# Performance work log

Measured on AMD Instinct MI355X. Metric: run time of the kernel, lower is better.

## Reference

```python
import jax, jax.numpy as jnp
import numpy as np

B, QL, VL, HID, NH, CH = 16, 512, 512, 1024, 4, 10
DIM = HID // NH  # 256


def setup_inputs() -> dict:
    key = jax.random.key(0)
    ks = jax.random.split(key, 16)
    n = lambda k, s, sc=0.02: jax.random.normal(k, s, jnp.float32) * sc
    return {
        "query": jax.random.normal(ks[0], (B, QL, HID), jnp.float32),
        "value": jax.random.normal(ks[1], (B, VL, HID), jnp.float32),
        "prev_attn": jax.nn.softmax(jax.random.normal(ks[2], (B * NH, VL), jnp.float32), axis=-1),
        "conv_w": n(ks[3], (CH, 1, 3)),          # conv1d weight (out, in, k)
        "conv_b": jnp.zeros((CH,), jnp.float32),
        "Wq": n(ks[4], (HID, HID)), "bq": jnp.zeros((HID,), jnp.float32),  # query_projection
        "Wv": n(ks[5], (HID, HID)),               # value_projection (no bias)
        "Wloc": n(ks[6], (CH, DIM)),              # loc_projection (no bias)
        "bias": jax.random.uniform(ks[7], (HID,), jnp.float32, -0.1, 0.1),
        "Wout": n(ks[8], (2 * HID, HID)), "bout": jnp.zeros((HID,), jnp.float32),
        "swq": n(ks[9], (DIM, DIM)), "sbq": jnp.zeros((DIM,), jnp.float32),
        "swk": n(ks[10], (DIM, DIM)), "sbk": jnp.zeros((DIM,), jnp.float32),
        "swv": n(ks[11], (DIM, DIM)), "sbv": jnp.zeros((DIM,), jnp.float32),
    }


def _forward(query, value, prev_attn, conv_w, conv_b, Wq, bq, Wv, Wloc, bias,
             Wout, bout, swq, sbq, swk, sbk, swv, sbv):
    # location energy: conv1d over prev alignment, then per-head linear
    conv = jax.lax.conv_general_dilated(
        prev_attn[:, None, :], conv_w, window_strides=(1,), padding=((1, 1),),
        dimension_numbers=("NCH", "OIH", "NCH")) + conv_b[None, :, None]  # (B*NH, CH, VL)
    conv = conv.reshape(B, NH, CH, VL).transpose(0, 1, 3, 2)              # (B, NH, VL, CH)
    loc = jnp.einsum("bhvc,cd->bhvd", conv, Wloc)                         # (B, NH, VL, DIM)
    loc = loc.transpose(0, 2, 1, 3).reshape(B, VL, HID)                   # (B, VL, HID)

    q = query @ Wq + bq                                                   # (B, QL, HID)
    v = value @ Wv + loc + bias                                           # (B, VL, HID)

    # split heads: (B, L, NH, DIM) -> (NH*B, L, DIM)
    qh = q.reshape(B, QL, NH, DIM).transpose(2, 0, 1, 3).reshape(NH * B, QL, DIM)
    vh = v.reshape(B, VL, NH, DIM).transpose(2, 0, 1, 3).reshape(NH * B, VL, DIM)

    # scaled dot-product attention with key = value = vh (intended call)
    qq = qh @ swq + sbq
    kk = vh @ swk + sbk
    vv = vh @ swv + sbv
    scores = jnp.einsum("nqd,nkd->nqk", qq, kk) / np.float32(np.sqrt(DIM))
    attn = jax.nn.softmax(scores, axis=-1)                                # (NH*B, QL, VL)
    ctx = jnp.einsum("nqk,nkd->nqd", attn, vv)

    # merge heads: (NH, B, QL, DIM) -> (B, QL, HID)
    ctx = ctx.reshape(NH, B, QL, DIM).transpose(1, 2, 0, 3).reshape(B, QL, HID)

    combined = jnp.concatenate([ctx, query], axis=2)                      # (B, QL, 2*HID)
    out = jnp.tanh(combined @ Wout + bout)                                # (B, QL, HID)
    return out, attn


def reference(query, value, prev_attn, conv_w, conv_b, Wq, bq, Wv, Wloc, bias,
              Wout, bout, swq, sbq, swk, sbk, swv, sbv):
    return _forward(query, value, prev_attn, conv_w, conv_b, Wq, bq, Wv, Wloc,
                    bias, Wout, bout, swq, sbq, swk, sbk, swv, sbv)
```

## Files before the change

### kernel.cpp

```cpp
#include <hip/hip_runtime.h>
#include <math.h>

#define B_   16
#define QL_  512
#define VL_  512
#define HID_ 1024
#define NH_  4
#define CH_  10
#define DIM_ 256

typedef __attribute__((ext_vector_type(4))) float f32x4;
typedef __attribute__((ext_vector_type(8))) short bf16x8;
typedef long long ll;

__device__ __forceinline__ ushort f2bf(float f) {
    union { float f; uint32_t u; } c; c.f = f;
    uint32_t u = c.u;
    u += 0x7fffu + ((u >> 16) & 1u);
    return (ushort)(u >> 16);
}

__device__ __forceinline__ void gload16(const void* g, void* l) {
    __builtin_amdgcn_global_load_lds((const __attribute__((address_space(1))) void*)g,
                                     (__attribute__((address_space(3))) void*)l,
                                     16, 0, 0);
}

__global__ __launch_bounds__(512)
void gemm8p(const ushort* __restrict__ A, const ushort* __restrict__ Bt,
            void* __restrict__ Cv, void* __restrict__ Cv2,
            const float* __restrict__ bias,
            int K, int lda, int ldb, int ldc,
            float post_scale, int flags)
{
    __shared__ ushort As[2][256 * 32];
    __shared__ ushort Bs[2][128 * 32];

    int gx = gridDim.x, nwg = gx * gridDim.y;
    int flat = blockIdx.y * gx + blockIdx.x;
    int q = nwg >> 3, r = nwg & 7;
    int xcd = flat & 7, idx = flat >> 3;
    int logical = (xcd < r ? xcd * (q + 1) : r * (q + 1) + (xcd - r) * q) + idx;
    int brow = (logical / gx) * 256;
    int bcol = (logical % gx) * 128;

    int t = threadIdx.x;
    int lane = t & 63, w = t >> 6;
    int wm = w >> 1, wn = w & 1;
    int wr = wm * 64, wc = wn * 64;

    int srow = t >> 2, slot = t & 3;
    int sk = ((slot ^ ((srow >> 1) & 3)) << 3);
    const ushort* gA0 = A  + (ll)(brow + srow) * lda + sk;
    const ushort* gA1 = A  + (ll)(brow + 128 + srow) * lda + sk;
    const ushort* gB  = Bt + (ll)(bcol + srow) * ldb + sk;

    f32x4 acc[4][4] = {};

    auto stage = [&](int buf, int k0) {
        gload16(gA0 + k0, &As[buf][t * 8]);
        gload16(gA1 + k0, &As[buf][4096 + t * 8]);
        gload16(gB  + k0, &Bs[buf][t * 8]);
    };

    int NT = K >> 5;
    stage(0, 0);
    __syncthreads();
    int cur = 0;
    int slotR = (lane >> 4) ^ ((lane >> 1) & 3);
    for (int tI = 0; tI < NT; ++tI) {
        const ushort* ab = &As[cur][(wr + (lane & 15)) * 32 + slotR * 8];
        const ushort* bb = &Bs[cur][(wc + (lane & 15)) * 32 + slotR * 8];

        bf16x8 af[4], b0, b1;
        #pragma unroll
        for (int m = 0; m < 4; ++m) af[m] = *(const bf16x8*)(ab + m * 512);
        b0 = *(const bf16x8*)(bb);
        b1 = *(const bf16x8*)(bb + 512);
        if (tI + 1 < NT) stage(cur ^ 1, (tI + 1) << 5);
        __builtin_amdgcn_s_barrier();
        __builtin_amdgcn_sched_barrier(0);
        __builtin_amdgcn_s_setprio(1);
        #pragma unroll
        for (int m = 0; m < 4; ++m) {
            acc[m][0] = __builtin_amdgcn_mfma_f32_16x16x32_bf16(af[m], b0, acc[m][0], 0, 0, 0);
            acc[m][1] = __builtin_amdgcn_mfma_f32_16x16x32_bf16(af[m], b1, acc[m][1], 0, 0, 0);
        }
        __builtin_amdgcn_s_setprio(0);
        __builtin_amdgcn_s_barrier();
        __builtin_amdgcn_sched_barrier(0);

        bf16x8 b2 = *(const bf16x8*)(bb + 1024);
        bf16x8 b3 = *(const bf16x8*)(bb + 1536);
        __builtin_amdgcn_s_setprio(1);
        #pragma unroll
        for (int m = 0; m < 4; ++m) {
            acc[m][2] = __builtin_amdgcn_mfma_f32_16x16x32_bf16(af[m], b2, acc[m][2], 0, 0, 0);
            acc[m][3] = __builtin_amdgcn_mfma_f32_16x16x32_bf16(af[m], b3, acc[m][3], 0, 0, 0);
        }
        __builtin_amdgcn_s_setprio(0);
        if (tI + 1 < NT)
            asm volatile("s_waitcnt vmcnt(0)" ::: "memory");
        __builtin_amdgcn_s_barrier();
        __builtin_amdgcn_sched_barrier(0);
        cur ^= 1;
    }

    float*  Cf = (float*)Cv;
    ushort* Cb = (ushort*)Cv;
    ushort* C2 = (ushort*)Cv2;
    #pragma unroll
    for (int m = 0; m < 4; ++m) {
        int r0 = brow + wr + m * 16 + (lane >> 4) * 4;
        #pragma unroll
        for (int n = 0; n < 4; ++n) {
            int c = bcol + wc + n * 16 + (lane & 15);
            float bv = bias ? bias[c] : 0.0f;
            float v0 = (acc[m][n][0] + bv) * post_scale;
            float v1 = (acc[m][n][1] + bv) * post_scale;
            float v2 = (acc[m][n][2] + bv) * post_scale;
            float v3 = (acc[m][n][3] + bv) * post_scale;
            if (flags & 2) { v0 = tanhf(v0); v1 = tanhf(v1); v2 = tanhf(v2); v3 = tanhf(v3); }
            if ((flags & 8) && c >= 1024) {
                ushort4 o;
                o.x = f2bf(v0); o.y = f2bf(v1); o.z = f2bf(v2); o.w = f2bf(v3);
                *(ushort4*)&C2[(ll)(c - 1024) * 8192 + r0] = o;
            } else if (flags & 1) {
                Cb[(ll)(r0 + 0) * ldc + c] = f2bf(v0);
                Cb[(ll)(r0 + 1) * ldc + c] = f2bf(v1);
                Cb[(ll)(r0 + 2) * ldc + c] = f2bf(v2);
                Cb[(ll)(r0 + 3) * ldc + c] = f2bf(v3);
            } else {
                Cf[(ll)(r0 + 0) * ldc + c] = v0;
                Cf[(ll)(r0 + 1) * ldc + c] = v1;
                Cf[(ll)(r0 + 2) * ldc + c] = v2;
                Cf[(ll)(r0 + 3) * ldc + c] = v3;
            }
        }
    }
}

__global__ __launch_bounds__(256)
void gemm_bf16(const ushort* __restrict__ A, const ushort* __restrict__ Bt,
               void* __restrict__ Cv, void* __restrict__ Cv2,
               const float* __restrict__ bias,
               int K, int lda, int ldb, int ldc,
               long long a1, long long a2, long long b1, long long b2,
               long long c1, long long c2, int WB,
               float post_scale, int flags)
{
    __shared__ ushort As[2][128 * 64];
    __shared__ ushort Bs[2][128 * 64];

    int z = blockIdx.z;
    int zm = z % WB, zd = z / WB;
    A  += a1 * zm + a2 * zd;
    Bt += b1 * zm + b2 * zd;
    long long coff = c1 * (long long)zm + c2 * (long long)zd;

    int gx = gridDim.x;
    int nwg = gx * gridDim.y;
    int flat = blockIdx.y * gx + blockIdx.x;
    int q = nwg >> 3, r = nwg & 7;
    int xcd = flat & 7, idx = flat >> 3;
    int logical = (xcd < r ? xcd * (q + 1) : r * (q + 1) + (xcd - r) * q) + idx;
    int brow = (logical / gx) * 128;
    int bcol = (logical % gx) * 128;

    int t = threadIdx.x;
    int lane = t & 63, w = t >> 6;
    int wr = (w >> 1) * 64, wc = (w & 1) * 64;

    int srow  = t >> 3;
    int sslot = t & 7;
    int sk = ((sslot ^ (srow & 7)) << 3);
    const ushort* gaBase = A  + (long long)(brow + srow) * lda + sk;
    const ushort* gbBase = Bt + (long long)(bcol + srow) * ldb + sk;

    f32x4 acc[4][4] = {};

    auto stage = [&](int buf, int k0) {
        ushort* la = &As[buf][t * 8];
        ushort* lb = &Bs[buf][t * 8];
        #pragma unroll
        for (int i = 0; i < 4; ++i) {
            gload16(gaBase + (long long)(i * 32) * lda + k0, la + i * 2048);
            gload16(gbBase + (long long)(i * 32) * ldb + k0, lb + i * 2048);
        }
    };

    int NT = K >> 6;
    stage(0, 0);
    int cur = 0;
    for (int tI = 0; tI < NT; ++tI) {
        if (tI + 1 < NT) {
            stage(cur ^ 1, (tI + 1) << 6);
            asm volatile("s_waitcnt vmcnt(8)" ::: "memory");
        } else {
            asm volatile("s_waitcnt vmcnt(0)" ::: "memory");
        }
        __builtin_amdgcn_s_barrier();
        __builtin_amdgcn_sched_barrier(0);

        #pragma unroll
        for (int kk = 0; kk < 2; ++kk) {
            int slot = ((kk << 2) + (lane >> 4)) ^ (lane & 7);
            const ushort* ab = &As[cur][(wr + (lane & 15)) * 64 + slot * 8];
            const ushort* bb = &Bs[cur][(wc + (lane & 15)) * 64 + slot * 8];
            bf16x8 af[4], bfr[4];
            #pragma unroll
            for (int m = 0; m < 4; ++m) af[m]  = *(const bf16x8*)(ab + m * 1024);
            #pragma unroll
            for (int n = 0; n < 4; ++n) bfr[n] = *(const bf16x8*)(bb + n * 1024);
            #pragma unroll
            for (int m = 0; m < 4; ++m)
                #pragma unroll
                for (int n = 0; n < 4; ++n)
                    acc[m][n] = __builtin_amdgcn_mfma_f32_16x16x32_bf16(af[m], bfr[n], acc[m][n], 0, 0, 0);
        }

        __builtin_amdgcn_s_barrier();
        __builtin_amdgcn_sched_barrier(0);
        cur ^= 1;
    }

    float*  Cf = (float*)Cv + coff;
    ushort* Cb = (ushort*)Cv + coff;
    ushort* C2 = (ushort*)Cv2;
    #pragma unroll
    for (int m = 0; m < 4; ++m) {
        int r0 = brow + wr + m * 16 + (lane >> 4) * 4;
        #pragma unroll
        for (int n = 0; n < 4; ++n) {
            int c = bcol + wc + n * 16 + (lane & 15);
            float bv = bias ? bias[c] : 0.0f;
            float v0 = (acc[m][n][0] + bv) * post_scale;
            float v1 = (acc[m][n][1] + bv) * post_scale;
            float v2 = (acc[m][n][2] + bv) * post_scale;
            float v3 = (acc[m][n][3] + bv) * post_scale;
            if (flags & 2) { v0 = tanhf(v0); v1 = tanhf(v1); v2 = tanhf(v2); v3 = tanhf(v3); }
            if ((flags & 8) && c >= 1024) {
                ushort4 o;
                o.x = f2bf(v0); o.y = f2bf(v1); o.z = f2bf(v2); o.w = f2bf(v3);
                *(ushort4*)&C2[(long long)(c - 1024) * 8192 + r0] = o;
            } else if (flags & 1) {
                Cb[(long long)(r0 + 0) * ldc + c] = f2bf(v0);
                Cb[(long long)(r0 + 1) * ldc + c] = f2bf(v1);
                Cb[(long long)(r0 + 2) * ldc + c] = f2bf(v2);
                Cb[(long long)(r0 + 3) * ldc + c] = f2bf(v3);
            } else {
                Cf[(long long)(r0 + 0) * ldc + c] = v0;
                Cf[(long long)(r0 + 1) * ldc + c] = v1;
                Cf[(long long)(r0 + 2) * ldc + c] = v2;
                Cf[(long long)(r0 + 3) * ldc + c] = v3;
            }
        }
    }
}

__global__ __launch_bounds__(512, 1)
void scores_softmax(const ushort* __restrict__ qq, const ushort* __restrict__ kk,
                    float* __restrict__ attn, ushort* __restrict__ attnb)
{
    __shared__ ushort As[128 * 32];
    __shared__ ushort Bs[512 * 32];
    __shared__ float redm[4][128];
    __shared__ float reds[4][128];

    int z = blockIdx.z;
    int b = z & 15, h = z >> 4;
    const ushort* Abase = qq + (ll)b * 524288 + h * 256;
    const ushort* Bbase = kk + (ll)b * 524288 + h * 256;
    float*  aout = attn  + (ll)z * 262144;
    ushort* bout = attnb + (ll)z * 262144;

    int brow = blockIdx.y * 128;

    int t = threadIdx.x;
    int lane = t & 63, w = t >> 6;
    int wr = (w >> 2) * 64;
    int wc = (w & 3) * 128;

    int srow = t >> 2, sslot = t & 3;
    int sk = ((sslot ^ ((srow >> 1) & 3)) << 3);
    const ushort* ga = Abase + (ll)(brow + srow) * 1024 + sk;
    const ushort* gb = Bbase + (ll)srow * 1024 + sk;

    f32x4 acc[4][8] = {};

    for (int k0 = 0; k0 < 256; k0 += 32) {
        gload16(ga + k0, &As[t * 8]);
        #pragma unroll
        for (int i = 0; i < 4; ++i)
            gload16(gb + (ll)(i * 128) * 1024 + k0, &Bs[t * 8 + i * 4096]);
        __syncthreads();

        int slot = (lane >> 4) ^ ((lane >> 1) & 3);
        const ushort* ab = &As[(wr + (lane & 15)) * 32 + slot * 8];
        const ushort* bb = &Bs[(wc + (lane & 15)) * 32 + slot * 8];
        bf16x8 af[4], bfr[8];
        #pragma unroll
        for (int m = 0; m < 4; ++m) af[m]  = *(const bf16x8*)(ab + m * 512);
        #pragma unroll
        for (int n = 0; n < 8; ++n) bfr[n] = *(const bf16x8*)(bb + n * 512);
        #pragma unroll
        for (int m = 0; m < 4; ++m)
            #pragma unroll
            for (int n = 0; n < 8; ++n)
                acc[m][n] = __builtin_amdgcn_mfma_f32_16x16x32_bf16(af[m], bfr[n], acc[m][n], 0, 0, 0);
        __syncthreads();
    }

    float rmax[4][4], rinv[4][4];
    #pragma unroll
    for (int m = 0; m < 4; ++m)
        #pragma unroll
        for (int j = 0; j < 4; ++j) {
            float pm = acc[m][0][j];
            #pragma unroll
            for (int n = 1; n < 8; ++n) pm = fmaxf(pm, acc[m][n][j]);
            pm = fmaxf(pm, __shfl_xor(pm, 1));
            pm = fmaxf(pm, __shfl_xor(pm, 2));
            pm = fmaxf(pm, __shfl_xor(pm, 4));
            pm = fmaxf(pm, __shfl_xor(pm, 8));
            if ((lane & 15) == 0)
                redm[w & 3][wr + m * 16 + (lane >> 4) * 4 + j] = pm;
        }
    __syncthreads();
    #pragma unroll
    for (int m = 0; m < 4; ++m)
        #pragma unroll
        for (int j = 0; j < 4; ++j) {
            int row = wr + m * 16 + (lane >> 4) * 4 + j;
            rmax[m][j] = fmaxf(fmaxf(redm[0][row], redm[1][row]),
                               fmaxf(redm[2][row], redm[3][row]));
        }
    #pragma unroll
    for (int m = 0; m < 4; ++m)
        #pragma unroll
        for (int j = 0; j < 4; ++j) {
            float ps = 0.f;
            #pragma unroll
            for (int n = 0; n < 8; ++n) {
                float e = __expf(acc[m][n][j] - rmax[m][j]);
                acc[m][n][j] = e;
                ps += e;
            }
            ps += __shfl_xor(ps, 1);
            ps += __shfl_xor(ps, 2);
            ps += __shfl_xor(ps, 4);
            ps += __shfl_xor(ps, 8);
            if ((lane & 15) == 0)
                reds[w & 3][wr + m * 16 + (lane >> 4) * 4 + j] = ps;
        }
    __syncthreads();
    #pragma unroll
    for (int m = 0; m < 4; ++m)
        #pragma unroll
        for (int j = 0; j < 4; ++j) {
            int row = wr + m * 16 + (lane >> 4) * 4 + j;
            rinv[m][j] = 1.0f / (reds[0][row] + reds[1][row] + reds[2][row] + reds[3][row]);
        }
    #pragma unroll
    for (int m = 0; m < 4; ++m) {
        int r0 = brow + wr + m * 16 + (lane >> 4) * 4;
        #pragma unroll
        for (int n = 0; n < 8; ++n) {
            int c = wc + n * 16 + (lane & 15);
            #pragma unroll
            for (int j = 0; j < 4; ++j) {
                float v = acc[m][n][j] * rinv[m][j];
                aout[(ll)(r0 + j) * 512 + c] = v;
                bout[(ll)(r0 + j) * 512 + c] = f2bf(v);
            }
        }
    }
}

__global__ __launch_bounds__(256)
void prep_acts(const float* __restrict__ query, const float* __restrict__ value,
               const float* __restrict__ prev, const float* __restrict__ cw,
               const float* __restrict__ cb,
               ushort* __restrict__ Acat, ushort* __restrict__ vext)
{
    int bI = blockIdx.x;
    if (bI < 16384) {
        const float* in = (bI < 8192) ? query : value;
        ushort* out = (bI < 8192) ? Acat : vext;
        int ld_out = (bI < 8192) ? 2048 : 1088;
        ll idx = (ll)(bI & 8191) * 256 + threadIdx.x;
        ll row = idx >> 8;
        int c4 = (int)(idx & 255) * 4;
        float4 v = *(const float4*)&in[row * 1024 + c4];
        ushort4 o;
        o.x = f2bf(v.x); o.y = f2bf(v.y); o.z = f2bf(v.z); o.w = f2bf(v.w);
        *(ushort4*)&out[row * ld_out + c4] = o;
    } else {
        int idx = (bI - 16384) * 256 + threadIdx.x;
        int row = idx >> 6, j = idx & 63;
        int b = row >> 9, l = row & 511;
        ushort v = 0;
        if (j < 40) {
            int h = j / 10, c = j - h * 10;
            const float* p = prev + (ll)(b * 4 + h) * VL_;
            float xm = (l > 0)       ? p[l - 1] : 0.f;
            float x0 = p[l];
            float xp = (l < VL_ - 1) ? p[l + 1] : 0.f;
            v = f2bf(xm * cw[c * 3 + 0] + x0 * cw[c * 3 + 1] + xp * cw[c * 3 + 2] + cb[c]);
        }
        vext[(ll)row * 1088 + 1024 + j] = v;
    }
}

__global__ __launch_bounds__(256)
void prep_w(const float* __restrict__ Wq, const float* __restrict__ Wv,
            ushort* __restrict__ Wqb, ushort* __restrict__ Wvb,
            const float* __restrict__ bq, const float* __restrict__ sbq, const float* __restrict__ swq,
            const float* __restrict__ bias, const float* __restrict__ sbk, const float* __restrict__ swk,
            const float* __restrict__ sbv, const float* __restrict__ swv,
            const float* __restrict__ Wloc,
            float* __restrict__ bqq, float* __restrict__ bkv,
            float* __restrict__ wlK, float* __restrict__ wlV)
{
    int bI = blockIdx.x;
    if (bI < 2048) {
        const float* in = (bI < 1024) ? Wq : Wv;
        ushort* out = (bI < 1024) ? Wqb : Wvb;
        ll idx = (ll)(bI & 1023) * 256 + threadIdx.x;
        ll row = idx >> 8;
        int c4 = (int)(idx & 255) * 4;
        float4 v = *(const float4*)&in[row * 1024 + c4];
        ushort4 o;
        o.x = f2bf(v.x); o.y = f2bf(v.y); o.z = f2bf(v.z); o.w = f2bf(v.w);
        *(ushort4*)&out[row * 1024 + c4] = o;
        return;
    }
    int idx = (bI - 2048) * 256 + threadIdx.x;
    if (idx < 1024) {
        int h = idx >> 8, d = idx & 255;
        float s = 0.f;
        for (int j = 0; j < 256; ++j) s += bq[h * 256 + j] * swq[j * 256 + d];
        bqq[idx] = s + sbq[d];
    } else if (idx < 3072) {
        int i = idx - 1024;
        int kv = i >> 10, ii = i & 1023;
        int h = ii >> 8, d = ii & 255;
        const float* sw = kv ? swv : swk;
        const float* sb = kv ? sbv : sbk;
        float s = 0.f;
        for (int j = 0; j < 256; ++j) s += bias[h * 256 + j] * sw[j * 256 + d];
        bkv[i] = s + sb[d];
    } else if (idx < 5632) {
        int i = idx - 3072; int c = i >> 8, d = i & 255;
        float s = 0.f;
        for (int j = 0; j < 256; ++j) s += Wloc[c * 256 + j] * swk[j * 256 + d];
        wlK[i] = s;
    } else if (idx < 8192) {
        int i = idx - 5632; int c = i >> 8, d = i & 255;
        float s = 0.f;
        for (int j = 0; j < 256; ++j) s += Wloc[c * 256 + j] * swv[j * 256 + d];
        wlV[i] = s;
    }
}

__global__ __launch_bounds__(256)
void transpose_cast(const float* __restrict__ in, ushort* __restrict__ out, int R, int C, int ld_out)
{
    __shared__ float tile[64][65];
    int r0 = blockIdx.y * 64, c0 = blockIdx.x * 64;
    int t = threadIdx.x;
    int tr = t >> 2, tc = (t & 3) * 16;
    const float* ip = in + (ll)(r0 + tr) * C + c0 + tc;
    #pragma unroll
    for (int i = 0; i < 4; ++i) {
        float4 v = *(const float4*)(ip + i * 4);
        tile[tr][tc + i * 4 + 0] = v.x;
        tile[tr][tc + i * 4 + 1] = v.y;
        tile[tr][tc + i * 4 + 2] = v.z;
        tile[tr][tc + i * 4 + 3] = v.w;
    }
    __syncthreads();
    int cl = t >> 2, rl = (t & 3) * 16;
    ushort* op = out + (ll)(c0 + cl) * ld_out + r0 + rl;
    #pragma unroll
    for (int i = 0; i < 16; ++i) op[i] = f2bf(tile[rl + i][cl]);
}

__global__ __launch_bounds__(256)
void sw3_transpose(const float* __restrict__ swq, const float* __restrict__ swk,
                   const float* __restrict__ swv, ushort* __restrict__ oq,
                   ushort* __restrict__ ok, ushort* __restrict__ ov)
{
    __shared__ float tile[64][65];
    const float* in = (blockIdx.z == 0) ? swq : (blockIdx.z == 1) ? swk : swv;
    ushort* out     = (blockIdx.z == 0) ? oq  : (blockIdx.z == 1) ? ok  : ov;
    int r0 = blockIdx.y * 64, c0 = blockIdx.x * 64;
    int t = threadIdx.x;
    int tr = t >> 2, tc = (t & 3) * 16;
    const float* ip = in + (ll)(r0 + tr) * 256 + c0 + tc;
    #pragma unroll
    for (int i = 0; i < 4; ++i) {
        float4 v = *(const float4*)(ip + i * 4);
        tile[tr][tc + i * 4 + 0] = v.x;
        tile[tr][tc + i * 4 + 1] = v.y;
        tile[tr][tc + i * 4 + 2] = v.z;
        tile[tr][tc + i * 4 + 3] = v.w;
    }
    __syncthreads();
    int cl = t >> 2, rl = (t & 3) * 16;
    ushort* op = out + (ll)(c0 + cl) * 256 + r0 + rl;
    #pragma unroll
    for (int i = 0; i < 16; ++i) op[i] = f2bf(tile[rl + i][cl]);
}

__global__ __launch_bounds__(256)
void btext_fill(const float* __restrict__ wlK, const float* __restrict__ wlV,
                ushort* __restrict__ btExt)
{
    int idx = blockIdx.x * 256 + threadIdx.x;
    int n = idx >> 6, j = idx & 63;
    ushort v = 0;
    if (j < 40) {
        int hp = j / 10, c = j - hp * 10;
        int nn = n & 1023;
        int h = nn >> 8, d = nn & 255;
        if (hp == h) {
            const float* wl = (n >= 1024) ? wlV : wlK;
            v = f2bf(wl[c * 256 + d]);
        }
    }
    btExt[(ll)n * 1088 + 1024 + j] = v;
}

extern "C" void kernel_launch(void* const* d_in, const int* in_sizes, int n_in,
                              void* d_out, int out_size, void* d_ws, size_t ws_size,
                              hipStream_t stream)
{
    (void)in_sizes; (void)n_in; (void)out_size; (void)ws_size;

    const float* query = (const float*)d_in[0];
    const float* value = (const float*)d_in[1];
    const float* prev  = (const float*)d_in[2];
    const float* convw = (const float*)d_in[3];
    const float* convb = (const float*)d_in[4];
    const float* Wq    = (const float*)d_in[5];
    const float* bq    = (const float*)d_in[6];
    const float* Wv    = (const float*)d_in[7];
    const float* Wloc  = (const float*)d_in[8];
    const float* bias  = (const float*)d_in[9];
    const float* Wout  = (const float*)d_in[10];
    const float* bout  = (const float*)d_in[11];
    const float* swq   = (const float*)d_in[12];
    const float* sbq   = (const float*)d_in[13];
    const float* swk   = (const float*)d_in[14];
    const float* sbk   = (const float*)d_in[15];
    const float* swv   = (const float*)d_in[16];
    const float* sbv   = (const float*)d_in[17];

    float* out_buf  = (float*)d_out;
    float* attn_buf = out_buf + (ll)B_ * QL_ * HID_;

    char* wsb = (char*)d_ws;
    ushort* vext   = (ushort*)(wsb + 0);
    ushort* WoutTb = (ushort*)(wsb + 0);
    ushort* kkb    = (ushort*)(wsb + 17825792);
    ushort* attnb  = (ushort*)(wsb + 34603008);
    ushort* Acat   = (ushort*)(wsb + 68157440);
    ushort* qqb    = (ushort*)(wsb + 101711872);
    ushort* vvT_b  = (ushort*)(wsb + 118489088);
    float*  bqq    = (float*)(wsb + 135266304);
    float*  bkv    = (float*)(wsb + 135270400);
    float*  wlK    = (float*)(wsb + 135278592);
    float*  wlV    = (float*)(wsb + 135288832);
    ushort* swqTb  = (ushort*)(wsb + 135299072);
    ushort* swkTb  = (ushort*)(wsb + 135430144);
    ushort* swvTb  = (ushort*)(wsb + 135561216);
    ushort* Wqb    = (ushort*)(wsb + 135692288);
    ushort* Wvb    = (ushort*)(wsb + 137789440);
    ushort* wqqTb  = (ushort*)(wsb + 139886592);
    ushort* btExt  = (ushort*)(wsb + 141983744);

    prep_acts<<<18432, 256, 0, stream>>>(query, value, prev, convw, convb, Acat + 1024, vext);
    prep_w<<<2080, 256, 0, stream>>>(Wq, Wv, Wqb, Wvb, bq, sbq, swq, bias, sbk, swk,
                                     sbv, swv, Wloc, bqq, bkv, wlK, wlV);
    sw3_transpose<<<dim3(4, 4, 3), 256, 0, stream>>>(swq, swk, swv, swqTb, swkTb, swvTb);

    gemm_bf16<<<dim3(8, 2, 4), 256, 0, stream>>>(swqTb, Wqb, wqqTb, nullptr, nullptr,
        256, 256, 1024, 1024, 0, 0, 0, 256, 0, 262144, 1, 1.0f, 1);
    gemm_bf16<<<dim3(8, 2, 8), 256, 0, stream>>>(swkTb, Wvb, btExt, nullptr, nullptr,
        256, 256, 1024, 1088, 0, 65536, 256, 0, 278528, 1114112, 4, 1.0f, 1);
    btext_fill<<<512, 256, 0, stream>>>(wlK, wlV, btExt);

    gemm8p<<<dim3(8, 32), 512, 0, stream>>>(Acat + 1024, wqqTb, qqb, nullptr, bqq,
        1024, 2048, 1024, 1024, 0.0625f, 1);

    gemm8p<<<dim3(16, 32), 512, 0, stream>>>(vext, btExt, kkb, vvT_b, bkv,
        1088, 1088, 1088, 1024, 1.0f, 1 | 8);

    transpose_cast<<<dim3(16, 32), 256, 0, stream>>>(Wout, WoutTb, 2048, 1024, 2048);

    scores_softmax<<<dim3(1, 4, 64), 512, 0, stream>>>(qqb, kkb, attn_buf, attnb);

    gemm_bf16<<<dim3(2, 4, 64), 256, 0, stream>>>(attnb, vvT_b, Acat, nullptr, nullptr,
        512, 512, 8192, 2048,
        262144, 4194304, 512, 2097152, 1048576, 256, 16, 1.0f, 1);

    gemm8p<<<dim3(8, 32), 512, 0, stream>>>(Acat, WoutTb, out_buf, nullptr, bout,
        2048, 2048, 2048, 1024, 1.0f, 2);
}
```

Before: 273.4 us.

## Enlarge GEMM tiles to 256x256 with K=64 stages and deeper prefetch

Replaces the 256x128, K=32 tile GEMM with a 256x256 tile using K=64 per stage, an 8-slot XOR swizzle, and four sub-phases per K step. The next stage's loads are issued before compute, with a partial vmcnt wait so two stages stay in flight. The goal is more operand reuse per LDS load and fewer barriers per FLOP. In exchange it uses 128KB of LDS and twice the accumulator registers, which lowers occupancy and halves the workgroup count (128 for the 1024-wide GEMMs), risking underfilled CUs.

```diff
diff --git a/kernel.cpp b/kernel.cpp
--- a/kernel.cpp
+++ b/kernel.cpp
@@ -27,14 +27,14 @@
 }
 
 __global__ __launch_bounds__(512)
-void gemm8p(const ushort* __restrict__ A, const ushort* __restrict__ Bt,
-            void* __restrict__ Cv, void* __restrict__ Cv2,
-            const float* __restrict__ bias,
-            int K, int lda, int ldb, int ldc,
-            float post_scale, int flags)
-{
-    __shared__ ushort As[2][256 * 32];
-    __shared__ ushort Bs[2][128 * 32];
+void gemm256p(const ushort* __restrict__ A, const ushort* __restrict__ Bt,
+              void* __restrict__ Cv, void* __restrict__ Cv2,
+              const float* __restrict__ bias,
+              int K, int lda, int ldb, int ldc,
+              float post_scale, int flags)
+{
+    __shared__ ushort As[2][256 * 64];
+    __shared__ ushort Bs[2][256 * 64];
 
     int gx = gridDim.x, nwg = gx * gridDim.y;
     int flat = blockIdx.y * gx + blockIdx.x;
@@ -42,67 +42,76 @@
     int xcd = flat & 7, idx = flat >> 3;
     int logical = (xcd < r ? xcd * (q + 1) : r * (q + 1) + (xcd - r) * q) + idx;
     int brow = (logical / gx) * 256;
-    int bcol = (logical % gx) * 128;
+    int bcol = (logical % gx) * 256;
 
     int t = threadIdx.x;
     int lane = t & 63, w = t >> 6;
-    int wm = w >> 1, wn = w & 1;
-    int wr = wm * 64, wc = wn * 64;
-
-    int srow = t >> 2, slot = t & 3;
-    int sk = ((slot ^ ((srow >> 1) & 3)) << 3);
-    const ushort* gA0 = A  + (ll)(brow + srow) * lda + sk;
-    const ushort* gA1 = A  + (ll)(brow + 128 + srow) * lda + sk;
-    const ushort* gB  = Bt + (ll)(bcol + srow) * ldb + sk;
-
-    f32x4 acc[4][4] = {};
+    int wm = w >> 2;
+    int wn = w & 3;
+
+    int srow = t >> 3, sslot = t & 7;
+    int sk = ((sslot ^ (srow & 7)) << 3);
+    const ushort* gaBase = A  + (ll)(brow + srow) * lda + sk;
+    const ushort* gbBase = Bt + (ll)(bcol + srow) * ldb + sk;
+
+    f32x4 acc[8][4] = {};
 
     auto stage = [&](int buf, int k0) {
-        gload16(gA0 + k0, &As[buf][t * 8]);
-        gload16(gA1 + k0, &As[buf][4096 + t * 8]);
-        gload16(gB  + k0, &Bs[buf][t * 8]);
+        #pragma unroll
+        for (int j = 0; j < 4; ++j) {
+            gload16(gaBase + (ll)(j * 64) * lda + k0, &As[buf][j * 4096 + t * 8]);
+            gload16(gbBase + (ll)(j * 64) * ldb + k0, &Bs[buf][j * 4096 + t * 8]);
+        }
     };
 
-    int NT = K >> 5;
+    int NT = K >> 6;
     stage(0, 0);
-    __syncthreads();
     int cur = 0;
-    int slotR = (lane >> 4) ^ ((lane >> 1) & 3);
     for (int tI = 0; tI < NT; ++tI) {
-        const ushort* ab = &As[cur][(wr + (lane & 15)) * 32 + slotR * 8];
-        const ushort* bb = &Bs[cur][(wc + (lane & 15)) * 32 + slotR * 8];
-
-        bf16x8 af[4], b0, b1;
-        #pragma unroll
-        for (int m = 0; m < 4; ++m) af[m] = *(const bf16x8*)(ab + m * 512);
-        b0 = *(const bf16x8*)(bb);
-        b1 = *(const bf16x8*)(bb + 512);
-        if (tI + 1 < NT) stage(cur ^ 1, (tI + 1) << 5);
+        if (tI + 1 < NT) {
+            stage(cur ^ 1, (tI + 1) << 6);
+            asm volatile("s_waitcnt vmcnt(8)" ::: "memory");
+        } else {
+            asm volatile("s_waitcnt vmcnt(0)" ::: "memory");
+        }
         __builtin_amdgcn_s_barrier();
         __builtin_amdgcn_sched_barrier(0);
-        __builtin_amdgcn_s_setprio(1);
-        #pragma unroll
-        for (int m = 0; m < 4; ++m) {
-            acc[m][0] = __builtin_amdgcn_mfma_f32_16x16x32_bf16(af[m], b0, acc[m][0], 0, 0, 0);
-            acc[m][1] = __builtin_amdgcn_mfma_f32_16x16x32_bf16(af[m], b1, acc[m][1], 0, 0, 0);
-        }
-        __builtin_amdgcn_s_setprio(0);
-        __builtin_amdgcn_s_barrier();
-        __builtin_amdgcn_sched_barrier(0);
-
-        bf16x8 b2 = *(const bf16x8*)(bb + 1024);
-        bf16x8 b3 = *(const bf16x8*)(bb + 1536);
-        __builtin_amdgcn_s_setprio(1);
-        #pragma unroll
-        for (int m = 0; m < 4; ++m) {
-            acc[m][2] = __builtin_amdgcn_mfma_f32_16x16x32_bf16(af[m], b2, acc[m][2], 0, 0, 0);
-            acc[m][3] = __builtin_amdgcn_mfma_f32_16x16x32_bf16(af[m], b3, acc[m][3], 0, 0, 0);
-        }
-        __builtin_amdgcn_s_setprio(0);
-        if (tI + 1 < NT)
-            asm volatile("s_waitcnt vmcnt(0)" ::: "memory");
-        __builtin_amdgcn_s_barrier();
-        __builtin_amdgcn_sched_barrier(0);
+
+        #pragma unroll
+        for (int p = 0; p < 4; ++p) {
+            int mq = p >> 1, nq = p & 1;
+            bf16x8 af[4][2], bfr[2][2];
+            #pragma unroll
+            for (int m = 0; m < 4; ++m) {
+                int R = wm * 128 + (mq * 4 + m) * 16 + (lane & 15);
+                #pragma unroll
+                for (int kf = 0; kf < 2; ++kf) {
+                    int g = kf * 4 + (lane >> 4);
+                    af[m][kf] = *(const bf16x8*)&As[cur][R * 64 + ((g ^ (lane & 7)) << 3)];
+                }
+            }
+            #pragma unroll
+            for (int n = 0; n < 2; ++n) {
+                int C = wn * 64 + (nq * 2 + n) * 16 + (lane & 15);
+                #pragma unroll
+                for (int kf = 0; kf < 2; ++kf) {
+                    int g = kf * 4 + (lane >> 4);
+                    bfr[n][kf] = *(const bf16x8*)&Bs[cur][C * 64 + ((g ^ (lane & 7)) << 3)];
+                }
+            }
+            __builtin_amdgcn_s_setprio(1);
+            #pragma unroll
+            for (int m = 0; m < 4; ++m)
+                #pragma unroll
+                for (int n = 0; n < 2; ++n)
+                    #pragma unroll
+                    for (int kf = 0; kf < 2; ++kf)
+                        acc[mq * 4 + m][nq * 2 + n] = __builtin_amdgcn_mfma_f32_16x16x32_bf16(
+                            af[m][kf], bfr[n][kf], acc[mq * 4 + m][nq * 2 + n], 0, 0, 0);
+            __builtin_amdgcn_s_setprio(0);
+            __builtin_amdgcn_s_barrier();
+            __builtin_amdgcn_sched_barrier(0);
+        }
         cur ^= 1;
     }
 
@@ -110,16 +119,16 @@
     ushort* Cb = (ushort*)Cv;
     ushort* C2 = (ushort*)Cv2;
     #pragma unroll
-    for (int m = 0; m < 4; ++m) {
-        int r0 = brow + wr + m * 16 + (lane >> 4) * 4;
-        #pragma unroll
-        for (int n = 0; n < 4; ++n) {
-            int c = bcol + wc + n * 16 + (lane & 15);
+    for (int mi = 0; mi < 8; ++mi) {
+        int r0 = brow + wm * 128 + mi * 16 + (lane >> 4) * 4;
+        #pragma unroll
+        for (int ni = 0; ni < 4; ++ni) {
+            int c = bcol + wn * 64 + ni * 16 + (lane & 15);
             float bv = bias ? bias[c] : 0.0f;
-            float v0 = (acc[m][n][0] + bv) * post_scale;
-            float v1 = (acc[m][n][1] + bv) * post_scale;
-            float v2 = (acc[m][n][2] + bv) * post_scale;
-            float v3 = (acc[m][n][3] + bv) * post_scale;
+            float v0 = (acc[mi][ni][0] + bv) * post_scale;
+            float v1 = (acc[mi][ni][1] + bv) * post_scale;
+            float v2 = (acc[mi][ni][2] + bv) * post_scale;
+            float v3 = (acc[mi][ni][3] + bv) * post_scale;
             if (flags & 2) { v0 = tanhf(v0); v1 = tanhf(v1); v2 = tanhf(v2); v3 = tanhf(v3); }
             if ((flags & 8) && c >= 1024) {
                 ushort4 o;
@@ -591,10 +600,10 @@
         256, 256, 1024, 1088, 0, 65536, 256, 0, 278528, 1114112, 4, 1.0f, 1);
     btext_fill<<<512, 256, 0, stream>>>(wlK, wlV, btExt);
 
-    gemm8p<<<dim3(8, 32), 512, 0, stream>>>(Acat + 1024, wqqTb, qqb, nullptr, bqq,
+    gemm256p<<<dim3(4, 32), 512, 0, stream>>>(Acat + 1024, wqqTb, qqb, nullptr, bqq,
         1024, 2048, 1024, 1024, 0.0625f, 1);
 
-    gemm8p<<<dim3(16, 32), 512, 0, stream>>>(vext, btExt, kkb, vvT_b, bkv,
+    gemm256p<<<dim3(8, 32), 512, 0, stream>>>(vext, btExt, kkb, vvT_b, bkv,
         1088, 1088, 1088, 1024, 1.0f, 1 | 8);
 
     transpose_cast<<<dim3(16, 32), 256, 0, stream>>>(Wout, WoutTb, 2048, 1024, 2048);
@@ -605,6 +614,6 @@
         512, 512, 8192, 2048,
         262144, 4194304, 512, 2097152, 1048576, 256, 16, 1.0f, 1);
 
-    gemm8p<<<dim3(8, 32), 512, 0, stream>>>(Acat, WoutTb, out_buf, nullptr, bout,
+    gemm256p<<<dim3(4, 32), 512, 0, stream>>>(Acat, WoutTb, out_buf, nullptr, bout,
         2048, 2048, 2048, 1024, 1.0f, 2);
 }
```

New measurement: 343.3 us. +25.5%, slower.

## Shrink GEMM tiles to 128x128 and double-buffer scores kernel with prefetch

Applied to the files above, without the earlier changes.

Replaces the 256x128, 8-wave gemm8p kernel with a 128x128, 4-wave gemm32 variant. The new kernel issues the next K-tile's global-to-LDS loads before computing the current one, waiting with a partial vmcnt, and drops the split-phase MFMA scheduling and setprio hints. The scores_softmax kernel gains double-buffered LDS so the next tile's loads overlap the current MFMAs. This trades larger-tile data reuse for twice as many workgroups and more overlap, and it doubles LDS use in scores_softmax.

```diff
diff --git a/kernel.cpp b/kernel.cpp
--- a/kernel.cpp
+++ b/kernel.cpp
@@ -26,14 +26,14 @@
                                      16, 0, 0);
 }
 
-__global__ __launch_bounds__(512)
-void gemm8p(const ushort* __restrict__ A, const ushort* __restrict__ Bt,
+__global__ __launch_bounds__(256)
+void gemm32(const ushort* __restrict__ A, const ushort* __restrict__ Bt,
             void* __restrict__ Cv, void* __restrict__ Cv2,
             const float* __restrict__ bias,
             int K, int lda, int ldb, int ldc,
             float post_scale, int flags)
 {
-    __shared__ ushort As[2][256 * 32];
+    __shared__ ushort As[2][128 * 32];
     __shared__ ushort Bs[2][128 * 32];
 
     int gx = gridDim.x, nwg = gx * gridDim.y;
@@ -41,66 +41,56 @@
     int q = nwg >> 3, r = nwg & 7;
     int xcd = flat & 7, idx = flat >> 3;
     int logical = (xcd < r ? xcd * (q + 1) : r * (q + 1) + (xcd - r) * q) + idx;
-    int brow = (logical / gx) * 256;
+    int brow = (logical / gx) * 128;
     int bcol = (logical % gx) * 128;
 
     int t = threadIdx.x;
     int lane = t & 63, w = t >> 6;
-    int wm = w >> 1, wn = w & 1;
-    int wr = wm * 64, wc = wn * 64;
-
-    int srow = t >> 2, slot = t & 3;
-    int sk = ((slot ^ ((srow >> 1) & 3)) << 3);
-    const ushort* gA0 = A  + (ll)(brow + srow) * lda + sk;
-    const ushort* gA1 = A  + (ll)(brow + 128 + srow) * lda + sk;
-    const ushort* gB  = Bt + (ll)(bcol + srow) * ldb + sk;
+    int wr = (w >> 1) * 64, wc = (w & 1) * 64;
+
+    int srow = t >> 2, sslot = t & 3;
+    int sk = ((sslot ^ ((srow >> 1) & 3)) << 3);
+    const ushort* gaBase = A  + (ll)(brow + srow) * lda + sk;
+    const ushort* gbBase = Bt + (ll)(bcol + srow) * ldb + sk;
 
     f32x4 acc[4][4] = {};
 
     auto stage = [&](int buf, int k0) {
-        gload16(gA0 + k0, &As[buf][t * 8]);
-        gload16(gA1 + k0, &As[buf][4096 + t * 8]);
-        gload16(gB  + k0, &Bs[buf][t * 8]);
+        ushort* la = &As[buf][t * 8];
+        ushort* lb = &Bs[buf][t * 8];
+        gload16(gaBase + k0, la);
+        gload16(gaBase + (ll)64 * lda + k0, la + 2048);
+        gload16(gbBase + k0, lb);
+        gload16(gbBase + (ll)64 * ldb + k0, lb + 2048);
     };
 
     int NT = K >> 5;
     stage(0, 0);
-    __syncthreads();
     int cur = 0;
     int slotR = (lane >> 4) ^ ((lane >> 1) & 3);
     for (int tI = 0; tI < NT; ++tI) {
+        if (tI + 1 < NT) {
+            stage(cur ^ 1, (tI + 1) << 5);
+            asm volatile("s_waitcnt vmcnt(4)" ::: "memory");
+        } else {
+            asm volatile("s_waitcnt vmcnt(0)" ::: "memory");
+        }
+        __builtin_amdgcn_s_barrier();
+        __builtin_amdgcn_sched_barrier(0);
+
         const ushort* ab = &As[cur][(wr + (lane & 15)) * 32 + slotR * 8];
         const ushort* bb = &Bs[cur][(wc + (lane & 15)) * 32 + slotR * 8];
-
-        bf16x8 af[4], b0, b1;
-        #pragma unroll
-        for (int m = 0; m < 4; ++m) af[m] = *(const bf16x8*)(ab + m * 512);
-        b0 = *(const bf16x8*)(bb);
-        b1 = *(const bf16x8*)(bb + 512);
-        if (tI + 1 < NT) stage(cur ^ 1, (tI + 1) << 5);
-        __builtin_amdgcn_s_barrier();
-        __builtin_amdgcn_sched_barrier(0);
-        __builtin_amdgcn_s_setprio(1);
-        #pragma unroll
-        for (int m = 0; m < 4; ++m) {
-            acc[m][0] = __builtin_amdgcn_mfma_f32_16x16x32_bf16(af[m], b0, acc[m][0], 0, 0, 0);
-            acc[m][1] = __builtin_amdgcn_mfma_f32_16x16x32_bf16(af[m], b1, acc[m][1], 0, 0, 0);
-        }
-        __builtin_amdgcn_s_setprio(0);
-        __builtin_amdgcn_s_barrier();
-        __builtin_amdgcn_sched_barrier(0);
-
-        bf16x8 b2 = *(const bf16x8*)(bb + 1024);
-        bf16x8 b3 = *(const bf16x8*)(bb + 1536);
-        __builtin_amdgcn_s_setprio(1);
-        #pragma unroll
-        for (int m = 0; m < 4; ++m) {
-            acc[m][2] = __builtin_amdgcn_mfma_f32_16x16x32_bf16(af[m], b2, acc[m][2], 0, 0, 0);
-            acc[m][3] = __builtin_amdgcn_mfma_f32_16x16x32_bf16(af[m], b3, acc[m][3], 0, 0, 0);
-        }
-        __builtin_amdgcn_s_setprio(0);
-        if (tI + 1 < NT)
-            asm volatile("s_waitcnt vmcnt(0)" ::: "memory");
+        bf16x8 af[4], bfr[4];
+        #pragma unroll
+        for (int m = 0; m < 4; ++m) af[m]  = *(const bf16x8*)(ab + m * 512);
+        #pragma unroll
+        for (int n = 0; n < 4; ++n) bfr[n] = *(const bf16x8*)(bb + n * 512);
+        #pragma unroll
+        for (int m = 0; m < 4; ++m)
+            #pragma unroll
+            for (int n = 0; n < 4; ++n)
+                acc[m][n] = __builtin_amdgcn_mfma_f32_16x16x32_bf16(af[m], bfr[n], acc[m][n], 0, 0, 0);
+
         __builtin_amdgcn_s_barrier();
         __builtin_amdgcn_sched_barrier(0);
         cur ^= 1;
@@ -262,8 +252,8 @@
 void scores_softmax(const ushort* __restrict__ qq, const ushort* __restrict__ kk,
                     float* __restrict__ attn, ushort* __restrict__ attnb)
 {
-    __shared__ ushort As[128 * 32];
-    __shared__ ushort Bs[512 * 32];
+    __shared__ ushort As[2][128 * 32];
+    __shared__ ushort Bs[2][512 * 32];
     __shared__ float redm[4][128];
     __shared__ float reds[4][128];
 
@@ -288,16 +278,29 @@
 
     f32x4 acc[4][8] = {};
 
-    for (int k0 = 0; k0 < 256; k0 += 32) {
-        gload16(ga + k0, &As[t * 8]);
+    auto stage = [&](int buf, int k0) {
+        gload16(ga + k0, &As[buf][t * 8]);
         #pragma unroll
         for (int i = 0; i < 4; ++i)
-            gload16(gb + (ll)(i * 128) * 1024 + k0, &Bs[t * 8 + i * 4096]);
-        __syncthreads();
+            gload16(gb + (ll)(i * 128) * 1024 + k0, &Bs[buf][t * 8 + i * 4096]);
+    };
+
+    int cur = 0;
+    stage(0, 0);
+    #pragma unroll
+    for (int tI = 0; tI < 8; ++tI) {
+        if (tI + 1 < 8) {
+            stage(cur ^ 1, (tI + 1) << 5);
+            asm volatile("s_waitcnt vmcnt(5)" ::: "memory");
+        } else {
+            asm volatile("s_waitcnt vmcnt(0)" ::: "memory");
+        }
+        __builtin_amdgcn_s_barrier();
+        __builtin_amdgcn_sched_barrier(0);
 
         int slot = (lane >> 4) ^ ((lane >> 1) & 3);
-        const ushort* ab = &As[(wr + (lane & 15)) * 32 + slot * 8];
-        const ushort* bb = &Bs[(wc + (lane & 15)) * 32 + slot * 8];
+        const ushort* ab = &As[cur][(wr + (lane & 15)) * 32 + slot * 8];
+        const ushort* bb = &Bs[cur][(wc + (lane & 15)) * 32 + slot * 8];
         bf16x8 af[4], bfr[8];
         #pragma unroll
         for (int m = 0; m < 4; ++m) af[m]  = *(const bf16x8*)(ab + m * 512);
@@ -308,7 +311,10 @@
             #pragma unroll
             for (int n = 0; n < 8; ++n)
                 acc[m][n] = __builtin_amdgcn_mfma_f32_16x16x32_bf16(af[m], bfr[n], acc[m][n], 0, 0, 0);
-        __syncthreads();
+
+        __builtin_amdgcn_s_barrier();
+        __builtin_amdgcn_sched_barrier(0);
+        cur ^= 1;
     }
 
     float rmax[4][4], rinv[4][4];
@@ -591,10 +597,10 @@
         256, 256, 1024, 1088, 0, 65536, 256, 0, 278528, 1114112, 4, 1.0f, 1);
     btext_fill<<<512, 256, 0, stream>>>(wlK, wlV, btExt);
 
-    gemm8p<<<dim3(8, 32), 512, 0, stream>>>(Acat + 1024, wqqTb, qqb, nullptr, bqq,
+    gemm32<<<dim3(8, 64), 256, 0, stream>>>(Acat + 1024, wqqTb, qqb, nullptr, bqq,
         1024, 2048, 1024, 1024, 0.0625f, 1);
 
-    gemm8p<<<dim3(16, 32), 512, 0, stream>>>(vext, btExt, kkb, vvT_b, bkv,
+    gemm32<<<dim3(16, 64), 256, 0, stream>>>(vext, btExt, kkb, vvT_b, bkv,
         1088, 1088, 1088, 1024, 1.0f, 1 | 8);
 
     transpose_cast<<<dim3(16, 32), 256, 0, stream>>>(Wout, WoutTb, 2048, 1024, 2048);
@@ -605,6 +611,6 @@
         512, 512, 8192, 2048,
         262144, 4194304, 512, 2097152, 1048576, 256, 16, 1.0f, 1);
 
-    gemm8p<<<dim3(8, 32), 512, 0, stream>>>(Acat, WoutTb, out_buf, nullptr, bout,
+    gemm32<<<dim3(8, 64), 256, 0, stream>>>(Acat, WoutTb, out_buf, nullptr, bout,
         2048, 2048, 2048, 1024, 1.0f, 2);
 }
```

Measured after the change: 281.7 us. 3.0% more time.
